# Kernel optimization log

Measured on AMD Instinct MI355X. Metric: run time of the kernel, lower is better.

Reference implementation:

```python
import jax, jax.numpy as jnp
import numpy as np
from functools import partial

B, IN, H, OUT, DEPTH = 4096, 1024, 2048, 1024, 8


def setup_inputs() -> dict:
    key = jax.random.key(0)
    ks = jax.random.split(key, 20)
    r = lambda k, shape: jax.random.normal(k, shape, dtype=jnp.float32)
    return {
        "x":  r(ks[0], (B, IN)),
        "W0": r(ks[1], (IN, H)) / np.sqrt(IN),  "b0": r(ks[2], (H,)) * 0.01,
        "W1": r(ks[3], (H, H)) / np.sqrt(H),    "b1": r(ks[4], (H,)) * 0.01,
        "cw1": r(ks[5], (DEPTH, H, H)), "cb1": r(ks[6], (H,)),
        "KW1": r(ks[7], (H, H)) / np.sqrt(H),  "Kb1": r(ks[8], (H,)) * 0.01,
        "W2": r(ks[9], (H, H)) / np.sqrt(H),   "b2": r(ks[10], (H,)) * 0.01,
        "cw2": r(ks[11], (DEPTH, H, H)), "cb2": r(ks[12], (H,)),
        "KW2": r(ks[13], (H, H)) / np.sqrt(H), "Kb2": r(ks[14], (H,)) * 0.01,
        "W3": r(ks[15], (H, OUT)) / np.sqrt(H), "b3": r(ks[16], (OUT,)) * 0.01,
    }


def _cosmic_processing(cw, batch, n_in, n_out):
    # state starts uniform over the n_in-dim 'cosmic' register, one per output j
    s0 = jnp.full((n_out, n_in), 1.0 / np.sqrt(n_in), dtype=cw.dtype)
    angles = cw[:, :, :3]  # (depth, n_out, 3): consciousness/intelligence/wisdom angles

    def step(s, ang):  # s: (n_out, n_in), ang: (n_out, 3)
        # circulant rotation: (M s)[i] = cos*s[i] - sin*s[i+1] + sin*s[i-1]
        for k in range(3):
            c = jnp.cos(ang[:, k])[:, None]
            si = jnp.sin(ang[:, k])[:, None]
            s = c * s - si * jnp.roll(s, -1, axis=1) + si * jnp.roll(s, 1, axis=1)
        return s, None

    s, _ = jax.lax.scan(step, s0, angles)
    prob = jnp.abs(s[:, 0]) ** 2  # (n_out,), sample-independent
    return jnp.broadcast_to(prob[None, :], (batch, n_out))


def _cosmic_layer(x, cw, cb, KW, Kb):
    classical = x @ KW + Kb
    cosmic = _cosmic_processing(cw, x.shape[0], x.shape[1], KW.shape[1])
    return jnp.tanh(classical + cosmic)


def reference(x, W0, b0, W1, b1, cw1, cb1, KW1, Kb1,
              W2, b2, cw2, cb2, KW2, Kb2, W3, b3):
    h = jax.nn.relu(x @ W0 + b0)
    h = jax.nn.relu(h @ W1 + b1)
    h = _cosmic_layer(h, cw1, cb1, KW1, Kb1)
    h = jax.nn.relu(h @ W2 + b2)
    h = _cosmic_layer(h, cw2, cb2, KW2, Kb2)
    return jax.nn.relu(h @ W3 + b3)
```

## Files before the change

kernel.cpp:

```cpp
#include <hip/hip_runtime.h>
#include <math.h>


typedef _Float16 f16;
typedef _Float16 f16x8 __attribute__((ext_vector_type(8)));
typedef _Float16 f16x4 __attribute__((ext_vector_type(4)));
typedef float f32x16 __attribute__((ext_vector_type(16)));

#define GLD16(gp, lp) __builtin_amdgcn_global_load_lds( \
    (const __attribute__((address_space(1))) unsigned int*)(gp), \
    (__attribute__((address_space(3))) unsigned int*)(lp), 16, 0, 0)

__global__ void cast_f32_f16(const float* __restrict__ in, f16* __restrict__ out, int n4) {
  int i = blockIdx.x * 256 + threadIdx.x;
  if (i < n4) {
    float4 v = ((const float4*)in)[i];
    f16x4 o = { (f16)v.x, (f16)v.y, (f16)v.z, (f16)v.w };
    ((f16x4*)out)[i] = o;
  }
}

struct TD { const float* src; f16* dst; int K; int N; };
struct TD6 { TD d[6]; };

__global__ void cast_transpose6(TD6 a) {
  TD d = a.d[blockIdx.z];
  int bx = blockIdx.x * 32, by = blockIdx.y * 32;
  if (bx >= d.N || by >= d.K) return;
  __shared__ float tile[32][33];
  int tx = threadIdx.x & 31, ty = threadIdx.x >> 5;
#pragma unroll
  for (int r = ty; r < 32; r += 8)
    tile[r][tx] = d.src[(size_t)(by + r) * d.N + bx + tx];
  __syncthreads();
#pragma unroll
  for (int r = ty; r < 32; r += 8)
    d.dst[(size_t)(bx + r) * d.K + by + tx] = (f16)tile[tx][r];
}

__global__ void cosmic_pp(const float* __restrict__ cw, float* __restrict__ pp, int H) {
  int i = blockIdx.x * 256 + threadIdx.x;
  if (i >= 8 * H) return;
  const float* a = cw + (size_t)i * H;
  pp[i] = cosf(a[0]) * cosf(a[1]) * cosf(a[2]);
}
__global__ void cosmic_fin(const float* __restrict__ pp, float* __restrict__ prob, int H) {
  int r = blockIdx.x * 256 + threadIdx.x;
  if (r >= H) return;
  float p = 1.0f;
#pragma unroll
  for (int d = 0; d < 8; ++d) p *= pp[d * H + r];
  prob[r] = p * p / (float)H;
}

template <int EPI, int BM>
__global__ __launch_bounds__(512, 2)
void gemm_f16(const f16* __restrict__ A, const f16* __restrict__ BT,
              const float* __restrict__ bias, const float* __restrict__ prob,
              f16* __restrict__ Ch, float* __restrict__ Cf,
              int M, int N, int K, int GX) {
  constexpr int ASZ = BM * 64;
  constexpr int BSZ = 128 * 64;
  constexpr int MB  = BM / 128;
  constexpr int RA  = BM / 64;
  __shared__ f16 lds[3 * (ASZ + BSZ)];
  f16* As = lds;
  f16* Bs = lds + 3 * ASZ;

  const int t = threadIdx.x;

  const int nwg = gridDim.x;
  const int bid = blockIdx.x;
  const int swz = (bid & 7) * (nwg >> 3) + (bid >> 3);
  const int bx = swz % GX;
  const int by = swz / GX;
  const int m0 = by * BM;
  const int n0 = bx * 128;

  auto stageA = [&](int kt, int buf, int q) {
    int F = q * 4096 + t * 8;
    int r = F >> 6, c = (F >> 3) & 7;
    const f16* src = A + (size_t)(m0 + r) * K + (kt << 6) + ((c ^ (r & 7)) << 3);
    GLD16(src, As + buf * ASZ + F);
  };
  auto stageB = [&](int kt, int buf, int q) {
    int F = q * 4096 + t * 8;
    int r = F >> 6, c = (F >> 3) & 7;
    const f16* src = BT + (size_t)(n0 + r) * K + (kt << 6) + ((c ^ (r & 7)) << 3);
    GLD16(src, Bs + buf * BSZ + F);
  };
  auto stage_all = [&](int kt, int buf) {
#pragma unroll
    for (int q = 0; q < RA; ++q) stageA(kt, buf, q);
#pragma unroll
    for (int q = 0; q < 2; ++q) stageB(kt, buf, q);
  };

  const int wave = t >> 6, lane = t & 63;
  const int wr = wave >> 1, wc = wave & 1;
  const int rc = lane & 31, hi = lane >> 5;

  f32x16 acc[MB][2] = {};

  auto kphase = [&](int cur, int p, int stage_kt, int sb) {
    const f16* Ab = As + cur * ASZ;
    const f16* Bb = Bs + cur * BSZ;
    const int cc = p * 2 + hi;
    f16x8 a[MB], b[2];
#pragma unroll
    for (int mb = 0; mb < MB; ++mb) {
      int row = wr * (BM / 4) + mb * 32 + rc;
      a[mb] = *(const f16x8*)&Ab[row * 64 + ((cc ^ (row & 7)) << 3)];
    }
#pragma unroll
    for (int nb = 0; nb < 2; ++nb) {
      int row = wc * 64 + nb * 32 + rc;
      b[nb] = *(const f16x8*)&Bb[row * 64 + ((cc ^ (row & 7)) << 3)];
    }
    if (stage_kt >= 0) {
      if (BM == 256) {
        stageA(stage_kt, sb, p);
        if (p < 2) stageB(stage_kt, sb, p);
      } else {
        if (p < 2) stageA(stage_kt, sb, p);
        else stageB(stage_kt, sb, p - 2);
      }
    }
    asm volatile("s_waitcnt lgkmcnt(0)" ::: "memory");
    __builtin_amdgcn_sched_barrier(0);
    __builtin_amdgcn_s_setprio(1);
#pragma unroll
    for (int mb = 0; mb < MB; ++mb)
#pragma unroll
      for (int nb = 0; nb < 2; ++nb)
        acc[mb][nb] = __builtin_amdgcn_mfma_f32_32x32x16_f16(a[mb], b[nb], acc[mb][nb], 0, 0, 0);
    __builtin_amdgcn_s_setprio(0);
    __builtin_amdgcn_sched_barrier(0);
  };

  const int nt = K >> 6;
  stage_all(0, 0);
  stage_all(1, 1);
  int cur = 0;
  for (int kt = 0; kt < nt; ++kt) {
    if (kt + 1 < nt) {
      if (BM == 256) asm volatile("s_waitcnt vmcnt(6)" ::: "memory");
      else           asm volatile("s_waitcnt vmcnt(4)" ::: "memory");
    } else {
      asm volatile("s_waitcnt vmcnt(0)" ::: "memory");
    }
    __builtin_amdgcn_s_barrier();
    int sb = cur + 2; if (sb >= 3) sb -= 3;
    const int skt = (kt + 2 < nt) ? (kt + 2) : -1;
#pragma unroll
    for (int p = 0; p < 4; ++p) kphase(cur, p, skt, sb);
    cur = (cur + 1 == 3) ? 0 : cur + 1;
  }

#pragma unroll
  for (int nb = 0; nb < 2; ++nb) {
    const int col = n0 + wc * 64 + nb * 32 + rc;
    float bn = bias[col];
    if (EPI == 1) bn += prob[col];
#pragma unroll
    for (int mb = 0; mb < MB; ++mb) {
      const int rbase = m0 + wr * (BM / 4) + mb * 32 + 4 * hi;
#pragma unroll
      for (int r = 0; r < 16; ++r) {
        const int row = rbase + (r & 3) + 8 * (r >> 2);
        float v = acc[mb][nb][r] + bn;
        if (EPI == 1) v = tanhf(v);
        else v = fmaxf(v, 0.0f);
        if (EPI == 2) Cf[(size_t)row * N + col] = v;
        else Ch[(size_t)row * N + col] = (f16)v;
      }
    }
  }
}

extern "C" void kernel_launch(void* const* d_in, const int* in_sizes, int n_in,
                              void* d_out, int out_size, void* d_ws, size_t ws_size,
                              hipStream_t stream) {
  const float* x   = (const float*)d_in[0];
  const float* W0  = (const float*)d_in[1];
  const float* b0  = (const float*)d_in[2];
  const float* W1  = (const float*)d_in[3];
  const float* b1  = (const float*)d_in[4];
  const float* cw1 = (const float*)d_in[5];
  const float* KW1 = (const float*)d_in[7];
  const float* Kb1 = (const float*)d_in[8];
  const float* W2  = (const float*)d_in[9];
  const float* b2  = (const float*)d_in[10];
  const float* cw2 = (const float*)d_in[11];
  const float* KW2 = (const float*)d_in[13];
  const float* Kb2 = (const float*)d_in[14];
  const float* W3  = (const float*)d_in[15];
  const float* b3  = (const float*)d_in[16];

  const int B = 4096, IN = 1024, H = 2048, OUT = 1024;

  char* ws = (char*)d_ws;
  size_t off = 0;
  auto alloc = [&](size_t bytes) {
    char* p = ws + off;
    off = (off + bytes + 255) & ~(size_t)255;
    return p;
  };
  f16* xh    = (f16*)alloc((size_t)B * IN * 2);
  f16* W0T   = (f16*)alloc((size_t)H * IN * 2);
  f16* W1T   = (f16*)alloc((size_t)H * H * 2);
  f16* KW1T  = (f16*)alloc((size_t)H * H * 2);
  f16* W2T   = (f16*)alloc((size_t)H * H * 2);
  f16* KW2T  = (f16*)alloc((size_t)H * H * 2);
  f16* W3T   = (f16*)alloc((size_t)OUT * H * 2);
  f16* hA    = (f16*)alloc((size_t)B * H * 2);
  f16* hB    = (f16*)alloc((size_t)B * H * 2);
  float* p1  = (float*)alloc((size_t)H * 4);
  float* p2  = (float*)alloc((size_t)H * 4);
  float* pp  = (float*)alloc((size_t)8 * H * 4);
  (void)ws_size;

  cast_f32_f16<<<(B * IN / 4 + 255) / 256, 256, 0, stream>>>(x, xh, B * IN / 4);

  TD6 td;
  td.d[0] = { W0,  W0T,  IN, H };
  td.d[1] = { W1,  W1T,  H,  H };
  td.d[2] = { KW1, KW1T, H,  H };
  td.d[3] = { W2,  W2T,  H,  H };
  td.d[4] = { KW2, KW2T, H,  H };
  td.d[5] = { W3,  W3T,  H,  OUT };
  cast_transpose6<<<dim3(H / 32, H / 32, 6), 256, 0, stream>>>(td);

  cosmic_pp<<<(8 * H + 255) / 256, 256, 0, stream>>>(cw1, pp, H);
  cosmic_fin<<<(H + 255) / 256, 256, 0, stream>>>(pp, p1, H);
  cosmic_pp<<<(8 * H + 255) / 256, 256, 0, stream>>>(cw2, pp, H);
  cosmic_fin<<<(H + 255) / 256, 256, 0, stream>>>(pp, p2, H);

  {
    int gx = H / 128, gy = B / 256;
    dim3 g(gx * gy);
    gemm_f16<0, 256><<<g, 512, 0, stream>>>(xh, W0T, b0,  nullptr, hA, nullptr, B, H, IN, gx);
    gemm_f16<0, 256><<<g, 512, 0, stream>>>(hA, W1T, b1,  nullptr, hB, nullptr, B, H, H,  gx);
    gemm_f16<1, 256><<<g, 512, 0, stream>>>(hB, KW1T, Kb1, p1,     hA, nullptr, B, H, H,  gx);
    gemm_f16<0, 256><<<g, 512, 0, stream>>>(hA, W2T, b2,  nullptr, hB, nullptr, B, H, H,  gx);
    gemm_f16<1, 256><<<g, 512, 0, stream>>>(hB, KW2T, Kb2, p2,     hA, nullptr, B, H, H,  gx);
  }
  {
    int gx = OUT / 128, gy = B / 128;
    dim3 g(gx * gy);
    gemm_f16<2, 128><<<g, 512, 0, stream>>>(hA, W3T, b3, nullptr, nullptr, (float*)d_out, B, OUT, H, gx);
  }
}
```

Baseline: 234.2 us.

## Vectorize cast-transpose and restructure GEMM k-loop to batch LDS reads before MFMAs

The weight cast-transpose kernel now loads float4 rows into a 32x64 tile and writes eight fp16 values per thread, cutting memory instructions and launched blocks. In the GEMM main loop, the per-phase interleaving of LDS fragment reads, global-to-LDS staging and MFMAs is replaced with one bulk issue of the next stage's prefetch, all four k-phase fragment reads, then all MFMAs. This removes the per-phase lgkmcnt waits and sched barriers but holds four phases of fragments in registers, raising register pressure, and gives up the fine-grained interleaving of loads with MFMA work.

```diff
diff --git a/kernel.cpp b/kernel.cpp
--- a/kernel.cpp
+++ b/kernel.cpp
@@ -25,17 +25,26 @@
 
 __global__ void cast_transpose6(TD6 a) {
   TD d = a.d[blockIdx.z];
-  int bx = blockIdx.x * 32, by = blockIdx.y * 32;
+  const int bx = blockIdx.x * 64;
+  const int by = blockIdx.y * 32;
   if (bx >= d.N || by >= d.K) return;
-  __shared__ float tile[32][33];
-  int tx = threadIdx.x & 31, ty = threadIdx.x >> 5;
-#pragma unroll
-  for (int r = ty; r < 32; r += 8)
-    tile[r][tx] = d.src[(size_t)(by + r) * d.N + bx + tx];
+  __shared__ float tile[32][68];
+  const int t = threadIdx.x;
+#pragma unroll
+  for (int pass = 0; pass < 2; ++pass) {
+    int idx = t + pass * 256;
+    int row = idx >> 4;
+    int c4  = (idx & 15) * 4;
+    float4 v = *(const float4*)&d.src[(size_t)(by + row) * d.N + bx + c4];
+    *(float4*)&tile[row][c4] = v;
+  }
   __syncthreads();
-#pragma unroll
-  for (int r = ty; r < 32; r += 8)
-    d.dst[(size_t)(bx + r) * d.K + by + tx] = (f16)tile[tx][r];
+  const int nl = t >> 2;
+  const int k8 = (t & 3) * 8;
+  f16x8 o;
+#pragma unroll
+  for (int j = 0; j < 8; ++j) o[j] = (f16)tile[k8 + j][nl];
+  *(f16x8*)&d.dst[(size_t)(bx + nl) * d.K + by + k8] = o;
 }
 
 __global__ void cosmic_pp(const float* __restrict__ cw, float* __restrict__ pp, int H) {
@@ -77,23 +86,20 @@
   const int m0 = by * BM;
   const int n0 = bx * 128;
 
-  auto stageA = [&](int kt, int buf, int q) {
-    int F = q * 4096 + t * 8;
-    int r = F >> 6, c = (F >> 3) & 7;
-    const f16* src = A + (size_t)(m0 + r) * K + (kt << 6) + ((c ^ (r & 7)) << 3);
-    GLD16(src, As + buf * ASZ + F);
-  };
-  auto stageB = [&](int kt, int buf, int q) {
-    int F = q * 4096 + t * 8;
-    int r = F >> 6, c = (F >> 3) & 7;
-    const f16* src = BT + (size_t)(n0 + r) * K + (kt << 6) + ((c ^ (r & 7)) << 3);
-    GLD16(src, Bs + buf * BSZ + F);
-  };
   auto stage_all = [&](int kt, int buf) {
-#pragma unroll
-    for (int q = 0; q < RA; ++q) stageA(kt, buf, q);
-#pragma unroll
-    for (int q = 0; q < 2; ++q) stageB(kt, buf, q);
+    const int k0 = kt << 6;
+#pragma unroll
+    for (int q = 0; q < RA; ++q) {
+      int F = q * 4096 + t * 8;
+      int r = F >> 6, c = (F >> 3) & 7;
+      GLD16(A + (size_t)(m0 + r) * K + k0 + ((c ^ (r & 7)) << 3), As + buf * ASZ + F);
+    }
+#pragma unroll
+    for (int q = 0; q < 2; ++q) {
+      int F = q * 4096 + t * 8;
+      int r = F >> 6, c = (F >> 3) & 7;
+      GLD16(BT + (size_t)(n0 + r) * K + k0 + ((c ^ (r & 7)) << 3), Bs + buf * BSZ + F);
+    }
   };
 
   const int wave = t >> 6, lane = t & 63;
@@ -101,42 +107,6 @@
   const int rc = lane & 31, hi = lane >> 5;
 
   f32x16 acc[MB][2] = {};
-
-  auto kphase = [&](int cur, int p, int stage_kt, int sb) {
-    const f16* Ab = As + cur * ASZ;
-    const f16* Bb = Bs + cur * BSZ;
-    const int cc = p * 2 + hi;
-    f16x8 a[MB], b[2];
-#pragma unroll
-    for (int mb = 0; mb < MB; ++mb) {
-      int row = wr * (BM / 4) + mb * 32 + rc;
-      a[mb] = *(const f16x8*)&Ab[row * 64 + ((cc ^ (row & 7)) << 3)];
-    }
-#pragma unroll
-    for (int nb = 0; nb < 2; ++nb) {
-      int row = wc * 64 + nb * 32 + rc;
-      b[nb] = *(const f16x8*)&Bb[row * 64 + ((cc ^ (row & 7)) << 3)];
-    }
-    if (stage_kt >= 0) {
-      if (BM == 256) {
-        stageA(stage_kt, sb, p);
-        if (p < 2) stageB(stage_kt, sb, p);
-      } else {
-        if (p < 2) stageA(stage_kt, sb, p);
-        else stageB(stage_kt, sb, p - 2);
-      }
-    }
-    asm volatile("s_waitcnt lgkmcnt(0)" ::: "memory");
-    __builtin_amdgcn_sched_barrier(0);
-    __builtin_amdgcn_s_setprio(1);
-#pragma unroll
-    for (int mb = 0; mb < MB; ++mb)
-#pragma unroll
-      for (int nb = 0; nb < 2; ++nb)
-        acc[mb][nb] = __builtin_amdgcn_mfma_f32_32x32x16_f16(a[mb], b[nb], acc[mb][nb], 0, 0, 0);
-    __builtin_amdgcn_s_setprio(0);
-    __builtin_amdgcn_sched_barrier(0);
-  };
 
   const int nt = K >> 6;
   stage_all(0, 0);
@@ -150,10 +120,37 @@
       asm volatile("s_waitcnt vmcnt(0)" ::: "memory");
     }
     __builtin_amdgcn_s_barrier();
-    int sb = cur + 2; if (sb >= 3) sb -= 3;
-    const int skt = (kt + 2 < nt) ? (kt + 2) : -1;
-#pragma unroll
-    for (int p = 0; p < 4; ++p) kphase(cur, p, skt, sb);
+    if (kt + 2 < nt) {
+      int sb = cur + 2; if (sb >= 3) sb -= 3;
+      stage_all(kt + 2, sb);
+    }
+
+    const f16* Ab = As + cur * ASZ;
+    const f16* Bb = Bs + cur * BSZ;
+    f16x8 a[4][MB], b[4][2];
+#pragma unroll
+    for (int p = 0; p < 4; ++p) {
+      const int cc = p * 2 + hi;
+#pragma unroll
+      for (int mb = 0; mb < MB; ++mb) {
+        int row = wr * (BM / 4) + mb * 32 + rc;
+        a[p][mb] = *(const f16x8*)&Ab[row * 64 + ((cc ^ (row & 7)) << 3)];
+      }
+#pragma unroll
+      for (int nb = 0; nb < 2; ++nb) {
+        int row = wc * 64 + nb * 32 + rc;
+        b[p][nb] = *(const f16x8*)&Bb[row * 64 + ((cc ^ (row & 7)) << 3)];
+      }
+    }
+    __builtin_amdgcn_s_setprio(1);
+#pragma unroll
+    for (int p = 0; p < 4; ++p)
+#pragma unroll
+      for (int mb = 0; mb < MB; ++mb)
+#pragma unroll
+        for (int nb = 0; nb < 2; ++nb)
+          acc[mb][nb] = __builtin_amdgcn_mfma_f32_32x32x16_f16(a[p][mb], b[p][nb], acc[mb][nb], 0, 0, 0);
+    __builtin_amdgcn_s_setprio(0);
     cur = (cur + 1 == 3) ? 0 : cur + 1;
   }
 
@@ -229,7 +226,7 @@
   td.d[3] = { W2,  W2T,  H,  H };
   td.d[4] = { KW2, KW2T, H,  H };
   td.d[5] = { W3,  W3T,  H,  OUT };
-  cast_transpose6<<<dim3(H / 32, H / 32, 6), 256, 0, stream>>>(td);
+  cast_transpose6<<<dim3(H / 64, H / 32, 6), 256, 0, stream>>>(td);
 
   cosmic_pp<<<(8 * H + 255) / 256, 256, 0, stream>>>(cw1, pp, H);
   cosmic_fin<<<(H + 255) / 256, 256, 0, stream>>>(pp, p1, H);
```

Result: slower. 248.2 us (+6.0%).
